# Optimization experiments

Measured on AMD Instinct MI355X. Metric: run time of the kernel, lower is better.

## Reference

```python
import jax, jax.numpy as jnp
import numpy as np

T, MEM, B, DM, N, D = 1024, 1024, 4, 1024, 16, 64
C = MEM + T
SCALE = 1.0 / D ** 0.5
LN_EPS = 1e-5


def _rel_shift(x):
    # x: [T, C, B, N] -> Transformer-XL relative shift
    t, c = x.shape[0], x.shape[1]
    zero_pad = jnp.zeros((t, 1) + x.shape[2:], x.dtype)
    x_padded = jnp.concatenate([zero_pad, x], axis=1)  # [T, C+1, B, N]
    x_padded = x_padded.reshape((c + 1, t) + x.shape[2:])
    return x_padded[1:].reshape(x.shape)


def setup_inputs() -> dict:
    key = jax.random.key(0)
    ks = jax.random.split(key, 8)
    h = jax.random.normal(ks[0], (T, B, DM), jnp.float32)
    m = jax.random.normal(ks[1], (MEM, B, DM), jnp.float32)
    r = jax.random.normal(ks[2], (C, DM), jnp.float32)
    # causal mask with memory: query i (global pos MEM+i) may attend to j <= MEM+i
    mask = (jnp.arange(C)[None, :] > (jnp.arange(T)[:, None] + MEM))[:, :, None]  # [T,C,1] bool, True=disallow
    W_qkv = jax.random.normal(ks[3], (DM, 3 * N * D), jnp.float32) * 0.02
    W_r = jax.random.normal(ks[4], (DM, N * D), jnp.float32) * 0.02
    W_o = jax.random.normal(ks[5], (N * D, DM), jnp.float32) * 0.02
    r_w_bias = jax.random.normal(ks[6], (N, D), jnp.float32)
    r_r_bias = jax.random.normal(ks[7], (N, D), jnp.float32)
    ln_gamma = jnp.ones((DM,), jnp.float32)
    ln_beta = jnp.zeros((DM,), jnp.float32)
    return {"h": h, "m": m, "r": r, "mask": mask, "W_qkv": W_qkv, "W_r": W_r,
            "W_o": W_o, "r_w_bias": r_w_bias, "r_r_bias": r_r_bias,
            "ln_gamma": ln_gamma, "ln_beta": ln_beta}


def reference(h, m, r, mask, W_qkv, W_r, W_o, r_w_bias, r_r_bias, ln_gamma, ln_beta):
    t, b = h.shape[0], h.shape[1]
    c = r.shape[0]
    cat = jnp.concatenate([m, h], axis=0)          # [C, B, DM]
    w_heads = cat @ W_qkv                           # [C, B, 3*N*D]
    w_q, w_k, w_v = jnp.split(w_heads, 3, axis=-1)
    w_q = w_q[-t:].reshape(t, b, N, D)              # [T,B,N,D]
    w_k = w_k.reshape(c, b, N, D)                   # [C,B,N,D]
    w_v = w_v.reshape(c, b, N, D)                   # [C,B,N,D]
    r_k = (r @ W_r).reshape(c, N, D)                # [C,N,D]
    AC = jnp.einsum('ibnd,jbnd->ijbn', w_q + r_w_bias, w_k)
    BD = jnp.einsum('ibnd,jnd->ijbn', w_q + r_r_bias, r_k)
    BD = _rel_shift(BD)
    score = (AC + BD) * SCALE                       # [T,C,B,N]
    score = jnp.where(mask[:, :, :, None], jnp.float32(-65000.0), score.astype(jnp.float32)).astype(score.dtype)
    prob = jax.nn.softmax(score, axis=1)
    vec = jnp.einsum('ijbn,jbnd->ibnd', prob, w_v).reshape(t, b, N * D)
    attn_out = vec @ W_o                            # [T,B,DM]
    x = h + attn_out
    mu = jnp.mean(x, axis=-1, keepdims=True)
    var = jnp.mean((x - mu) ** 2, axis=-1, keepdims=True)
    return (x - mu) * jax.lax.rsqrt(var + LN_EPS) * ln_gamma + ln_beta
```

## Files before the change

### kernel.cpp

```cpp
#include <hip/hip_runtime.h>
#include <stdint.h>

#define T_LEN 1024
#define MEM_LEN 1024
#define C_LEN 2048
#define B_SZ 4
#define DM_ 1024
#define NH 16
#define HD 64

typedef __attribute__((ext_vector_type(8))) short short8;
typedef __attribute__((ext_vector_type(4))) float f32x4;
typedef __attribute__((ext_vector_type(4))) unsigned short ushort4v;
typedef __attribute__((ext_vector_type(4))) float float4v;

__device__ __forceinline__ unsigned short f2bf(float f) {
  union { float f; unsigned int u; } v; v.f = f;
  unsigned int r = v.u + 0x7fffu + ((v.u >> 16) & 1u);
  return (unsigned short)(r >> 16);
}
__device__ __forceinline__ float bf2f(unsigned short b) {
  union { unsigned int u; float f; } v; v.u = ((unsigned int)b) << 16;
  return v.f;
}
__device__ __forceinline__ f32x4 mfma16(short8 a, short8 b, f32x4 c) {
  return __builtin_amdgcn_mfma_f32_16x16x32_bf16(a, b, c, 0, 0, 0);
}

__global__ void k_cat_convert(const float* __restrict__ m, const float* __restrict__ h,
                              unsigned short* __restrict__ outB) {
  int idx = blockIdx.x * 256 + threadIdx.x;
  const int MQ = (MEM_LEN * B_SZ * DM_) / 4;
  float4v v;
  if (idx < MQ) v = ((const float4v*)m)[idx];
  else          v = ((const float4v*)h)[idx - MQ];
  ushort4v o;
  o.x = f2bf(v.x); o.y = f2bf(v.y); o.z = f2bf(v.z); o.w = f2bf(v.w);
  ((ushort4v*)outB)[idx] = o;
}

__global__ void k_f32_to_bf16(const float* __restrict__ in, unsigned short* __restrict__ outB, int nq) {
  int idx = blockIdx.x * 256 + threadIdx.x;
  if (idx >= nq) return;
  float4v v = ((const float4v*)in)[idx];
  ushort4v o;
  o.x = f2bf(v.x); o.y = f2bf(v.y); o.z = f2bf(v.z); o.w = f2bf(v.w);
  ((ushort4v*)outB)[idx] = o;
}

__global__ void k_transpose_bf16(const float* __restrict__ in, unsigned short* __restrict__ out,
                                 int R, int Ccols) {
  __shared__ float tile[32][33];
  int c0 = blockIdx.x * 32, r0 = blockIdx.y * 32;
  int tx = threadIdx.x & 31, ty = threadIdx.x >> 5;
#pragma unroll
  for (int p = 0; p < 4; ++p)
    tile[ty + 8 * p][tx] = in[(size_t)(r0 + ty + 8 * p) * Ccols + c0 + tx];
  __syncthreads();
#pragma unroll
  for (int p = 0; p < 4; ++p)
    out[(size_t)(c0 + ty + 8 * p) * R + r0 + tx] = f2bf(tile[tx][ty + 8 * p]);
}

template <int EPI>
__global__ __launch_bounds__(256) void k_gemm(const unsigned short* __restrict__ A,
                                              const unsigned short* __restrict__ BT,
                                              void* __restrict__ Cout, int M, int N, int K,
                                              int ldc, int col0) {
  __shared__ unsigned short As[128 * 64];
  __shared__ unsigned short Bs[128 * 64];
  const int tid = threadIdx.x;
  const int w = tid >> 6, l = tid & 63;
  const int wm = w >> 1, wn = w & 1;
  const int lg = l >> 4, lr = l & 15;
  const int gx = gridDim.x;
  const int pid = blockIdx.y * gx + blockIdx.x;
  const int xcd = pid & 7;
  const int idx = pid >> 3;
  const int cb = idx % gx;
  const int rb = (idx / gx) * 8 + xcd;
  const int m0 = rb * 128, n0 = cb * 128;
  f32x4 acc[4][4] = {};
  const int lrow8 = l >> 3;
  const int scol = (l & 7) * 8;
  const unsigned short* Abase = A + (size_t)m0 * K;
  const unsigned short* Bbase = BT + (size_t)n0 * K;
  for (int kt = 0; kt < K; kt += 64) {
    __syncthreads();
#pragma unroll
    for (int q = 0; q < 4; ++q) {
      int chunk = w * 4 + q;
      int row = chunk * 8 + lrow8;
      __builtin_amdgcn_global_load_lds(
          (const __attribute__((address_space(1))) void*)(Abase + (size_t)row * K + kt + scol),
          (__attribute__((address_space(3))) void*)(As + chunk * 512), 16, 0, 0);
      __builtin_amdgcn_global_load_lds(
          (const __attribute__((address_space(1))) void*)(Bbase + (size_t)row * K + kt + scol),
          (__attribute__((address_space(3))) void*)(Bs + chunk * 512), 16, 0, 0);
    }
    __syncthreads();
#pragma unroll
    for (int ks = 0; ks < 2; ++ks) {
      short8 a[4], bb[4];
#pragma unroll
      for (int mi = 0; mi < 4; ++mi)
        a[mi] = *(const short8*)&As[(wm * 64 + mi * 16 + lr) * 64 + ks * 32 + lg * 8];
#pragma unroll
      for (int ni = 0; ni < 4; ++ni)
        bb[ni] = *(const short8*)&Bs[(wn * 64 + ni * 16 + lr) * 64 + ks * 32 + lg * 8];
#pragma unroll
      for (int mi = 0; mi < 4; ++mi)
#pragma unroll
        for (int ni = 0; ni < 4; ++ni)
          acc[mi][ni] = mfma16(a[mi], bb[ni], acc[mi][ni]);
    }
  }
#pragma unroll
  for (int mi = 0; mi < 4; ++mi)
#pragma unroll
    for (int ni = 0; ni < 4; ++ni)
#pragma unroll
      for (int r = 0; r < 4; ++r) {
        int row = m0 + wm * 64 + mi * 16 + lg * 4 + r;
        int col = col0 + n0 + wn * 64 + ni * 16 + lr;
        if (EPI == 0)
          ((unsigned short*)Cout)[(size_t)row * ldc + col] = f2bf(acc[mi][ni][r]);
        else
          ((float*)Cout)[(size_t)row * ldc + col] = acc[mi][ni][r];
      }
}

__global__ void k_vt(const unsigned short* __restrict__ wheads, unsigned short* __restrict__ VT) {
  __shared__ unsigned short tile[64][72];
  int c0 = blockIdx.x * 64;
  int n = blockIdx.y, b = blockIdx.z;
  int t = threadIdx.x;
#pragma unroll
  for (int p = 0; p < 16; ++p) {
    int idx = p * 256 + t;
    int r = idx >> 6, d = idx & 63;
    tile[d][r] = wheads[(size_t)((c0 + r) * 4 + b) * 3072 + 2048 + n * 64 + d];
  }
  __syncthreads();
#pragma unroll
  for (int p = 0; p < 16; ++p) {
    int idx = p * 256 + t;
    int d = idx >> 6, c = idx & 63;
    VT[(size_t)((b * 16 + n) * 64 + d) * 2048 + c0 + c] = tile[d][c];
  }
}

__global__ void k_repack(const unsigned short* __restrict__ wheads,
                         const unsigned short* __restrict__ RkG,
                         unsigned short* __restrict__ Kp,
                         unsigned short* __restrict__ Qp,
                         unsigned short* __restrict__ Rkp) {
  int gid = blockIdx.x * 256 + threadIdx.x;
  const int NK = (B_SZ * NH * C_LEN * HD) / 8;
  const int NQ = (B_SZ * NH * T_LEN * HD) / 8;
  if (gid < NK) {
    int d0 = (gid & 7) * 8;
    int c  = (gid >> 3) & 2047;
    int n  = (gid >> 14) & 15;
    int b  = gid >> 18;
    short8 v = *(const short8*)&wheads[(size_t)(c * 4 + b) * 3072 + 1024 + n * 64 + d0];
    *(short8*)&Kp[(size_t)gid * 8] = v;
  } else if (gid < NK + NQ) {
    int g2 = gid - NK;
    int d0 = (g2 & 7) * 8;
    int t  = (g2 >> 3) & 1023;
    int n  = (g2 >> 13) & 15;
    int b  = g2 >> 17;
    short8 v = *(const short8*)&wheads[(size_t)((MEM_LEN + t) * 4 + b) * 3072 + n * 64 + d0];
    *(short8*)&Qp[(size_t)g2 * 8] = v;
  } else {
    int g3 = gid - NK - NQ;
    int d0 = (g3 & 7) * 8;
    int c  = (g3 >> 3) & 2047;
    int n  = g3 >> 14;
    short8 v = *(const short8*)&RkG[(size_t)c * 1024 + n * 64 + d0];
    *(short8*)&Rkp[(size_t)g3 * 8] = v;
  }
}

__global__ void k_bias_dots(const unsigned short* __restrict__ Kp,
                            const unsigned short* __restrict__ Rkp,
                            const float* __restrict__ rwb, const float* __restrict__ rrb,
                            float* __restrict__ uk, float* __restrict__ vr) {
  int gid = blockIdx.x * 256 + threadIdx.x;
  if (gid < B_SZ * NH * C_LEN) {
    int bn = gid >> 11;
    int n = bn & 15;
    const unsigned short* kp = Kp + (size_t)gid * 64;
    float s = 0.f;
#pragma unroll
    for (int q = 0; q < 8; ++q) {
      short8 v = *(const short8*)&kp[q * 8];
#pragma unroll
      for (int e = 0; e < 8; ++e)
        s += bf2f((unsigned short)v[e]) * rwb[n * 64 + q * 8 + e];
    }
    uk[gid] = s;
  } else {
    int g2 = gid - B_SZ * NH * C_LEN;
    int n = g2 >> 11;
    const unsigned short* rp = Rkp + (size_t)g2 * 64;
    float s = 0.f;
#pragma unroll
    for (int q = 0; q < 8; ++q) {
      short8 v = *(const short8*)&rp[q * 8];
#pragma unroll
      for (int e = 0; e < 8; ++e)
        s += bf2f((unsigned short)v[e]) * rrb[n * 64 + q * 8 + e];
    }
    vr[g2] = s;
  }
}

__device__ __forceinline__ void stage_tile(const unsigned short* __restrict__ Kbase,
                                           const unsigned short* __restrict__ Vbase,
                                           unsigned short* ksBuf, unsigned short* vsBuf,
                                           int j0, int tid) {
#pragma unroll
  for (int q = 0; q < 2; ++q) {
    int chunk = q * 256 + tid;
    int row = chunk >> 3;
    int slot = chunk & 7;
    int ss = slot ^ (row & 7);
    __builtin_amdgcn_global_load_lds(
        (const __attribute__((address_space(1))) void*)(Kbase + (size_t)(j0 + row) * 64 + ss * 8),
        (__attribute__((address_space(3))) void*)(ksBuf + chunk * 8), 16, 0, 0);
    __builtin_amdgcn_global_load_lds(
        (const __attribute__((address_space(1))) void*)(Vbase + (size_t)row * 2048 + j0 + ss * 8),
        (__attribute__((address_space(3))) void*)(vsBuf + chunk * 8), 16, 0, 0);
  }
}

__global__ __launch_bounds__(256) void k_attn(const unsigned short* __restrict__ Qp,
                                              const unsigned short* __restrict__ Kp,
                                              const unsigned short* __restrict__ VT,
                                              const unsigned short* __restrict__ Rkp,
                                              const float* __restrict__ uk,
                                              const float* __restrict__ vr,
                                              float* __restrict__ po,
                                              float* __restrict__ psumG) {
  __shared__ __align__(16) unsigned short Ks[2][64 * 64];
  __shared__ __align__(16) unsigned short Vs[2][64 * 64];
  __shared__ unsigned short P[4][16][72];
  const int tid = threadIdx.x;
  const int w = tid >> 6, l = tid & 63;
  const int lg = l >> 4, lr = l & 15;
  const int L = blockIdx.x;
  const int bnlo = L & 7;
  const int rest = L >> 3;
  const int bnhi = rest / 48;
  const int inner = rest - bnhi * 48;
  const int xt = inner / 3;
  const int s  = inner - xt * 3;
  const int bn = bnhi * 8 + bnlo;
  const int i0 = xt * 64;
  const int n = bn & 15, b = bn >> 4;
  const int wrow = i0 + w * 16;

  const int ntile = xt + 17;
  const int t0 = (s * ntile) / 3;
  const int t1 = ((s + 1) * ntile) / 3;

  const unsigned short* Kbase = Kp + (size_t)bn * 2048 * 64;
  const unsigned short* Vbase = VT + (size_t)bn * 64 * 2048;
  const unsigned short* Rkbase = Rkp + (size_t)n * 2048 * 64;

  short8 aq0, aq1;
  {
    const unsigned short* qp = Qp + (size_t)(bn * 1024 + wrow + lr) * 64 + lg * 8;
    aq0 = *(const short8*)qp;
    aq1 = *(const short8*)(qp + 32);
  }
  float psum[4];
  f32x4 o[4];
#pragma unroll
  for (int r = 0; r < 4; ++r) psum[r] = 0.f;
#pragma unroll
  for (int df = 0; df < 4; ++df) o[df] = (f32x4){0.f, 0.f, 0.f, 0.f};

  const float* ukp = uk + (size_t)bn * 2048;
  const float* vrp = vr + (size_t)n * 2048;

  stage_tile(Kbase, Vbase, Ks[0], Vs[0], t0 * 64, tid);
  stage_tile(Kbase, Vbase, Ks[1], Vs[1], (t0 + 1) * 64, tid);

  const float EXPC = 0.18033688011112042f;

  for (int jt = t0; jt < t1; ++jt) {
    const int j0 = jt * 64;
    const int cur = (jt - t0) & 1;
    if (jt + 1 < t1) { asm volatile("s_waitcnt vmcnt(4)" ::: "memory"); }
    else             { asm volatile("s_waitcnt vmcnt(0)" ::: "memory"); }
    __builtin_amdgcn_s_barrier();

    f32x4 sac[4];
#pragma unroll
    for (int jf = 0; jf < 4; ++jf) sac[jf] = (f32x4){0.f, 0.f, 0.f, 0.f};
#pragma unroll
    for (int jf = 0; jf < 4; ++jf) {
      int row = jf * 16 + lr;
      int rx = row & 7;
      short8 k0 = *(const short8*)&Ks[cur][row * 64 + ((lg ^ rx) * 8)];
      short8 k1 = *(const short8*)&Ks[cur][row * 64 + (((4 + lg) ^ rx) * 8)];
      sac[jf] = mfma16(aq0, k0, sac[jf]);
      sac[jf] = mfma16(aq1, k1, sac[jf]);
    }
    const int kbw = j0 + 1008 - i0 - w * 16;
    f32x4 gb[5];
#pragma unroll
    for (int jg = 0; jg < 5; ++jg) {
      int rowK = kbw + jg * 16 + lr;
      short8 b0 = {}, b1 = {};
      float vrv = 0.f;
      if (rowK < C_LEN) {
        const unsigned short* rp = Rkbase + (size_t)rowK * 64 + lg * 8;
        b0 = *(const short8*)rp;
        b1 = *(const short8*)(rp + 32);
        vrv = vrp[rowK];
      }
      f32x4 g = (f32x4){0.f, 0.f, 0.f, 0.f};
      g = mfma16(aq0, b0, g);
      g = mfma16(aq1, b1, g);
#pragma unroll
      for (int r = 0; r < 4; ++r) g[r] += vrv;
      gb[jg] = g;
    }
    float ukv[4];
#pragma unroll
    for (int jf = 0; jf < 4; ++jf) ukv[jf] = ukp[j0 + jf * 16 + lr];
    float p[4][4];
#pragma unroll
    for (int r = 0; r < 4; ++r) {
      const int R = lg * 4 + r;
      const int delta = lr + 15 - R;
      const int src = (l & 48) | (delta & 15);
      float v0 = __shfl(gb[0][r], src);
      float v1 = __shfl(gb[1][r], src);
      float v2 = __shfl(gb[2][r], src);
      float v3 = __shfl(gb[3][r], src);
      float v4 = __shfl(gb[4][r], src);
      const bool hi = delta >= 16;
      float bd0 = hi ? v1 : v0;
      float bd1 = hi ? v2 : v1;
      float bd2 = hi ? v3 : v2;
      float bd3 = hi ? v4 : v3;
      const int jlim = i0 + w * 16 + R + MEM_LEN;
      int j = j0 + lr;
      p[0][r] = (j > jlim) ? 0.f : exp2f((sac[0][r] + bd0 + ukv[0]) * EXPC);
      j += 16;
      p[1][r] = (j > jlim) ? 0.f : exp2f((sac[1][r] + bd1 + ukv[1]) * EXPC);
      j += 16;
      p[2][r] = (j > jlim) ? 0.f : exp2f((sac[2][r] + bd2 + ukv[2]) * EXPC);
      j += 16;
      p[3][r] = (j > jlim) ? 0.f : exp2f((sac[3][r] + bd3 + ukv[3]) * EXPC);
    }
#pragma unroll
    for (int jf = 0; jf < 4; ++jf)
#pragma unroll
      for (int r = 0; r < 4; ++r) psum[r] += p[jf][r];
#pragma unroll
    for (int jf = 0; jf < 4; ++jf)
#pragma unroll
      for (int r = 0; r < 4; ++r)
        P[w][lg * 4 + r][jf * 16 + lr] = f2bf(p[jf][r]);
#pragma unroll
    for (int ks = 0; ks < 2; ++ks) {
      short8 ap = *(const short8*)&P[w][lr][ks * 32 + lg * 8];
#pragma unroll
      for (int df = 0; df < 4; ++df) {
        int row = df * 16 + lr;
        int rx = row & 7;
        short8 vv = *(const short8*)&Vs[cur][row * 64 + (((ks * 4 + lg) ^ rx) * 8)];
        o[df] = mfma16(ap, vv, o[df]);
      }
    }
    __builtin_amdgcn_s_barrier();
    if (jt + 2 < t1)
      stage_tile(Kbase, Vbase, Ks[cur], Vs[cur], (jt + 2) * 64, tid);
  }
  const int pbase = (bn * 16 + xt) * 3 + s;
  float* poB = po + (size_t)pbase * 4096;
#pragma unroll
  for (int r = 0; r < 4; ++r) {
    float v = psum[r];
    v += __shfl_xor(v, 1);
    v += __shfl_xor(v, 2);
    v += __shfl_xor(v, 4);
    v += __shfl_xor(v, 8);
    if (lr == 0) psumG[pbase * 64 + w * 16 + lg * 4 + r] = v;
  }
#pragma unroll
  for (int df = 0; df < 4; ++df)
#pragma unroll
    for (int r = 0; r < 4; ++r)
      poB[(w * 16 + lg * 4 + r) * 64 + df * 16 + lr] = o[df][r];
}

__global__ __launch_bounds__(256) void k_ared(const float* __restrict__ po,
                                              const float* __restrict__ psumG,
                                              unsigned short* __restrict__ vec) {
  const int idx = blockIdx.x;
  const int tid = threadIdx.x;
  const int bn = idx >> 4, xt = idx & 15;
  const int b = bn >> 4, n = bn & 15;
  __shared__ float rs[64];
  if (tid < 64) {
    const float* q = psumG + idx * 192;
    rs[tid] = q[tid] + q[tid + 64] + q[tid + 128];
  }
  __syncthreads();
  const float4v* p0 = (const float4v*)(po + (size_t)(idx * 3 + 0) * 4096);
  const float4v* p1 = (const float4v*)(po + (size_t)(idx * 3 + 1) * 4096);
  const float4v* p2 = (const float4v*)(po + (size_t)(idx * 3 + 2) * 4096);
#pragma unroll
  for (int k = 0; k < 4; ++k) {
    int e = tid + k * 256;
    int row = e >> 4, d4 = e & 15;
    float4v a = p0[e], bb = p1[e], c = p2[e];
    float inv = 1.f / rs[row];
    int t = xt * 64 + row;
    ushort4v ov;
    ov.x = f2bf((a.x + bb.x + c.x) * inv);
    ov.y = f2bf((a.y + bb.y + c.y) * inv);
    ov.z = f2bf((a.z + bb.z + c.z) * inv);
    ov.w = f2bf((a.w + bb.w + c.w) * inv);
    *(ushort4v*)&vec[(size_t)(t * 4 + b) * 1024 + n * 64 + d4 * 4] = ov;
  }
}

__global__ __launch_bounds__(256) void k_ln(const float* __restrict__ xg, const float* __restrict__ h,
                                            const float* __restrict__ gamma, const float* __restrict__ beta,
                                            float* __restrict__ out) {
  const int row = blockIdx.x;
  const int t = threadIdx.x;
  __shared__ float red1[4], red2[4];
  float4v xv = ((const float4v*)(xg + (size_t)row * 1024))[t];
  float4v hv = ((const float4v*)(h + (size_t)row * 1024))[t];
  float x0 = xv.x + hv.x, x1 = xv.y + hv.y, x2 = xv.z + hv.z, x3 = xv.w + hv.w;
  float s = x0 + x1 + x2 + x3;
#pragma unroll
  for (int off = 1; off < 64; off <<= 1) s += __shfl_xor(s, off);
  if ((t & 63) == 0) red1[t >> 6] = s;
  __syncthreads();
  float mean = (red1[0] + red1[1] + red1[2] + red1[3]) * (1.f / 1024.f);
  float d0 = x0 - mean, d1 = x1 - mean, d2 = x2 - mean, d3 = x3 - mean;
  float q = d0 * d0 + d1 * d1 + d2 * d2 + d3 * d3;
#pragma unroll
  for (int off = 1; off < 64; off <<= 1) q += __shfl_xor(q, off);
  if ((t & 63) == 0) red2[t >> 6] = q;
  __syncthreads();
  float var = (red2[0] + red2[1] + red2[2] + red2[3]) * (1.f / 1024.f);
  float rs = rsqrtf(var + 1e-5f);
  float4v gv = ((const float4v*)gamma)[t];
  float4v bv = ((const float4v*)beta)[t];
  float4v ov;
  ov.x = d0 * rs * gv.x + bv.x;
  ov.y = d1 * rs * gv.y + bv.y;
  ov.z = d2 * rs * gv.z + bv.z;
  ov.w = d3 * rs * gv.w + bv.w;
  ((float4v*)(out + (size_t)row * 1024))[t] = ov;
}

extern "C" void kernel_launch(void* const* d_in, const int* in_sizes, int n_in,
                              void* d_out, int out_size, void* d_ws, size_t ws_size,
                              hipStream_t stream) {
  (void)in_sizes; (void)n_in; (void)out_size; (void)ws_size;
  const float* h    = (const float*)d_in[0];
  const float* m    = (const float*)d_in[1];
  const float* r    = (const float*)d_in[2];
  const float* Wqkv = (const float*)d_in[4];
  const float* Wr   = (const float*)d_in[5];
  const float* Wo   = (const float*)d_in[6];
  const float* rwb  = (const float*)d_in[7];
  const float* rrb  = (const float*)d_in[8];
  const float* gam  = (const float*)d_in[9];
  const float* bet  = (const float*)d_in[10];
  float* out = (float*)d_out;

  char* ws = (char*)d_ws;
  unsigned short* catB   = (unsigned short*)(ws + 0);
  unsigned short* WqkvT  = (unsigned short*)(ws + 16777216);
  unsigned short* WrT    = (unsigned short*)(ws + 23068672);
  unsigned short* WoT    = (unsigned short*)(ws + 25165824);
  unsigned short* wheads = (unsigned short*)(ws + 27262976);
  unsigned short* RkG    = (unsigned short*)(ws + 77594624);
  unsigned short* VT     = (unsigned short*)(ws + 81788928);
  float* uk              = (float*)(ws + 98566144);
  float* vr              = (float*)(ws + 99090432);
  unsigned short* vec    = (unsigned short*)(ws + 99221504);
  float* xbuf            = (float*)(ws + 107610112);
  unsigned short* rB     = (unsigned short*)(ws + 124387328);
  unsigned short* Kp     = (unsigned short*)(ws + 128581632);
  unsigned short* Qp     = (unsigned short*)(ws + 145358848);
  unsigned short* Rkp    = (unsigned short*)(ws + 153747456);

  float* po    = (float*)(ws + 27262976);
  float* psumG = (float*)(ws + 124387328);

  hipLaunchKernelGGL(k_cat_convert, dim3(8192), dim3(256), 0, stream, m, h, catB);
  hipLaunchKernelGGL(k_f32_to_bf16, dim3(2048), dim3(256), 0, stream, r, rB, 524288);
  hipLaunchKernelGGL(k_transpose_bf16, dim3(96, 32), dim3(256), 0, stream, Wqkv, WqkvT, 1024, 3072);
  hipLaunchKernelGGL(k_transpose_bf16, dim3(32, 32), dim3(256), 0, stream, Wr, WrT, 1024, 1024);
  hipLaunchKernelGGL(k_transpose_bf16, dim3(32, 32), dim3(256), 0, stream, Wo, WoT, 1024, 1024);
  hipLaunchKernelGGL(k_gemm<0>, dim3(16, 64), dim3(256), 0, stream,
                     catB, WqkvT + (size_t)1024 * 1024, (void*)wheads, 8192, 2048, 1024, 3072, 1024);
  hipLaunchKernelGGL(k_gemm<0>, dim3(8, 32), dim3(256), 0, stream,
                     catB + (size_t)4096 * 1024, WqkvT, (void*)(wheads + (size_t)4096 * 3072),
                     4096, 1024, 1024, 3072, 0);
  hipLaunchKernelGGL(k_gemm<0>, dim3(8, 16), dim3(256), 0, stream, rB, WrT, (void*)RkG, 2048, 1024, 1024, 1024, 0);
  hipLaunchKernelGGL(k_vt, dim3(32, 16, 4), dim3(256), 0, stream, wheads, VT);
  hipLaunchKernelGGL(k_repack, dim3(7168), dim3(256), 0, stream, wheads, RkG, Kp, Qp, Rkp);
  hipLaunchKernelGGL(k_bias_dots, dim3(640), dim3(256), 0, stream, Kp, Rkp, rwb, rrb, uk, vr);
  hipLaunchKernelGGL(k_attn, dim3(3072), dim3(256), 0, stream, Qp, Kp, VT, Rkp, uk, vr, po, psumG);
  hipLaunchKernelGGL(k_ared, dim3(1024), dim3(256), 0, stream, po, psumG, vec);
  hipLaunchKernelGGL(k_gemm<1>, dim3(8, 32), dim3(256), 0, stream, vec, WoT, (void*)xbuf, 4096, 1024, 1024, 1024, 0);
  hipLaunchKernelGGL(k_ln, dim3(4096), dim3(256), 0, stream, xbuf, h, gam, bet, out);
}
```

Before: 359.1 us.

## Fuse head-major repacking into GEMM epilogues and store attention partials as bf16

The QKV and R projection GEMMs now write K, V, Q and R_k straight into per-head [b,n,c,d] layouts from their epilogues. This removes the separate k_repack kernel and the intermediate wheads/RkG buffers, along with one full read and write of those tensors. The attention kernel's split-KV partial outputs are also stored as bf16 instead of fp32, halving that traffic into the reduction kernel at some cost in accumulation precision. The epilogue stores are scalar 2-byte writes scattered by head, which may coalesce worse than before.

```diff
diff --git a/kernel.cpp b/kernel.cpp
--- a/kernel.cpp
+++ b/kernel.cpp
@@ -62,11 +62,11 @@
     out[(size_t)(c0 + ty + 8 * p) * R + r0 + tx] = f2bf(tile[tx][ty + 8 * p]);
 }
 
-template <int EPI>
+template <int MODE>
 __global__ __launch_bounds__(256) void k_gemm(const unsigned short* __restrict__ A,
                                               const unsigned short* __restrict__ BT,
-                                              void* __restrict__ Cout, int M, int N, int K,
-                                              int ldc, int col0) {
+                                              void* __restrict__ out1, void* __restrict__ out2,
+                                              int M, int N, int K, int ldc) {
   __shared__ unsigned short As[128 * 64];
   __shared__ unsigned short Bs[128 * 64];
   const int tid = threadIdx.x;
@@ -122,24 +122,38 @@
 #pragma unroll
       for (int r = 0; r < 4; ++r) {
         int row = m0 + wm * 64 + mi * 16 + lg * 4 + r;
-        int col = col0 + n0 + wn * 64 + ni * 16 + lr;
-        if (EPI == 0)
-          ((unsigned short*)Cout)[(size_t)row * ldc + col] = f2bf(acc[mi][ni][r]);
-        else
-          ((float*)Cout)[(size_t)row * ldc + col] = acc[mi][ni][r];
+        int cc = n0 + wn * 64 + ni * 16 + lr;
+        float val = acc[mi][ni][r];
+        if (MODE == 1) {
+          ((float*)out1)[(size_t)row * ldc + cc] = val;
+        } else if (MODE == 2) {
+          int nn = (cc & 1023) >> 6, d = cc & 63;
+          int c = row >> 2, b = row & 3;
+          size_t addr = ((size_t)((b * 16 + nn) * 2048 + c)) * 64 + d;
+          unsigned short* dst = (cc < 1024) ? (unsigned short*)out1 : (unsigned short*)out2;
+          dst[addr] = f2bf(val);
+        } else if (MODE == 3) {
+          int nn = cc >> 6, d = cc & 63;
+          int t = row >> 2, b = row & 3;
+          ((unsigned short*)out1)[((size_t)((b * 16 + nn) * 1024 + t)) * 64 + d] = f2bf(val);
+        } else {
+          int nn = cc >> 6, d = cc & 63;
+          ((unsigned short*)out1)[((size_t)(nn * 2048 + row)) * 64 + d] = f2bf(val);
+        }
       }
 }
 
-__global__ void k_vt(const unsigned short* __restrict__ wheads, unsigned short* __restrict__ VT) {
+__global__ void k_vt(const unsigned short* __restrict__ Vp, unsigned short* __restrict__ VT) {
   __shared__ unsigned short tile[64][72];
   int c0 = blockIdx.x * 64;
   int n = blockIdx.y, b = blockIdx.z;
   int t = threadIdx.x;
+  const unsigned short* src = Vp + ((size_t)((b * 16 + n) * 2048 + c0)) * 64;
 #pragma unroll
   for (int p = 0; p < 16; ++p) {
     int idx = p * 256 + t;
     int r = idx >> 6, d = idx & 63;
-    tile[d][r] = wheads[(size_t)((c0 + r) * 4 + b) * 3072 + 2048 + n * 64 + d];
+    tile[d][r] = src[(size_t)r * 64 + d];
   }
   __syncthreads();
 #pragma unroll
@@ -147,39 +161,6 @@
     int idx = p * 256 + t;
     int d = idx >> 6, c = idx & 63;
     VT[(size_t)((b * 16 + n) * 64 + d) * 2048 + c0 + c] = tile[d][c];
-  }
-}
-
-__global__ void k_repack(const unsigned short* __restrict__ wheads,
-                         const unsigned short* __restrict__ RkG,
-                         unsigned short* __restrict__ Kp,
-                         unsigned short* __restrict__ Qp,
-                         unsigned short* __restrict__ Rkp) {
-  int gid = blockIdx.x * 256 + threadIdx.x;
-  const int NK = (B_SZ * NH * C_LEN * HD) / 8;
-  const int NQ = (B_SZ * NH * T_LEN * HD) / 8;
-  if (gid < NK) {
-    int d0 = (gid & 7) * 8;
-    int c  = (gid >> 3) & 2047;
-    int n  = (gid >> 14) & 15;
-    int b  = gid >> 18;
-    short8 v = *(const short8*)&wheads[(size_t)(c * 4 + b) * 3072 + 1024 + n * 64 + d0];
-    *(short8*)&Kp[(size_t)gid * 8] = v;
-  } else if (gid < NK + NQ) {
-    int g2 = gid - NK;
-    int d0 = (g2 & 7) * 8;
-    int t  = (g2 >> 3) & 1023;
-    int n  = (g2 >> 13) & 15;
-    int b  = g2 >> 17;
-    short8 v = *(const short8*)&wheads[(size_t)((MEM_LEN + t) * 4 + b) * 3072 + n * 64 + d0];
-    *(short8*)&Qp[(size_t)g2 * 8] = v;
-  } else {
-    int g3 = gid - NK - NQ;
-    int d0 = (g3 & 7) * 8;
-    int c  = (g3 >> 3) & 2047;
-    int n  = g3 >> 14;
-    short8 v = *(const short8*)&RkG[(size_t)c * 1024 + n * 64 + d0];
-    *(short8*)&Rkp[(size_t)g3 * 8] = v;
   }
 }
 
@@ -242,7 +223,7 @@
                                               const unsigned short* __restrict__ Rkp,
                                               const float* __restrict__ uk,
                                               const float* __restrict__ vr,
-                                              float* __restrict__ po,
+                                              unsigned short* __restrict__ po,
                                               float* __restrict__ psumG) {
   __shared__ __align__(16) unsigned short Ks[2][64 * 64];
   __shared__ __align__(16) unsigned short Vs[2][64 * 64];
@@ -384,7 +365,7 @@
       stage_tile(Kbase, Vbase, Ks[cur], Vs[cur], (jt + 2) * 64, tid);
   }
   const int pbase = (bn * 16 + xt) * 3 + s;
-  float* poB = po + (size_t)pbase * 4096;
+  unsigned short* poB = po + (size_t)pbase * 4096;
 #pragma unroll
   for (int r = 0; r < 4; ++r) {
     float v = psum[r];
@@ -398,10 +379,10 @@
   for (int df = 0; df < 4; ++df)
 #pragma unroll
     for (int r = 0; r < 4; ++r)
-      poB[(w * 16 + lg * 4 + r) * 64 + df * 16 + lr] = o[df][r];
-}
-
-__global__ __launch_bounds__(256) void k_ared(const float* __restrict__ po,
+      poB[(w * 16 + lg * 4 + r) * 64 + df * 16 + lr] = f2bf(o[df][r]);
+}
+
+__global__ __launch_bounds__(256) void k_ared(const unsigned short* __restrict__ po,
                                               const float* __restrict__ psumG,
                                               unsigned short* __restrict__ vec) {
   const int idx = blockIdx.x;
@@ -414,21 +395,21 @@
     rs[tid] = q[tid] + q[tid + 64] + q[tid + 128];
   }
   __syncthreads();
-  const float4v* p0 = (const float4v*)(po + (size_t)(idx * 3 + 0) * 4096);
-  const float4v* p1 = (const float4v*)(po + (size_t)(idx * 3 + 1) * 4096);
-  const float4v* p2 = (const float4v*)(po + (size_t)(idx * 3 + 2) * 4096);
+  const ushort4v* p0 = (const ushort4v*)(po + (size_t)(idx * 3 + 0) * 4096);
+  const ushort4v* p1 = (const ushort4v*)(po + (size_t)(idx * 3 + 1) * 4096);
+  const ushort4v* p2 = (const ushort4v*)(po + (size_t)(idx * 3 + 2) * 4096);
 #pragma unroll
   for (int k = 0; k < 4; ++k) {
     int e = tid + k * 256;
     int row = e >> 4, d4 = e & 15;
-    float4v a = p0[e], bb = p1[e], c = p2[e];
+    ushort4v a = p0[e], bb = p1[e], c = p2[e];
     float inv = 1.f / rs[row];
     int t = xt * 64 + row;
     ushort4v ov;
-    ov.x = f2bf((a.x + bb.x + c.x) * inv);
-    ov.y = f2bf((a.y + bb.y + c.y) * inv);
-    ov.z = f2bf((a.z + bb.z + c.z) * inv);
-    ov.w = f2bf((a.w + bb.w + c.w) * inv);
+    ov.x = f2bf((bf2f(a.x) + bf2f(bb.x) + bf2f(c.x)) * inv);
+    ov.y = f2bf((bf2f(a.y) + bf2f(bb.y) + bf2f(c.y)) * inv);
+    ov.z = f2bf((bf2f(a.z) + bf2f(bb.z) + bf2f(c.z)) * inv);
+    ov.w = f2bf((bf2f(a.w) + bf2f(bb.w) + bf2f(c.w)) * inv);
     *(ushort4v*)&vec[(size_t)(t * 4 + b) * 1024 + n * 64 + d4 * 4] = ov;
   }
 }
@@ -487,8 +468,8 @@
   unsigned short* WqkvT  = (unsigned short*)(ws + 16777216);
   unsigned short* WrT    = (unsigned short*)(ws + 23068672);
   unsigned short* WoT    = (unsigned short*)(ws + 25165824);
-  unsigned short* wheads = (unsigned short*)(ws + 27262976);
-  unsigned short* RkG    = (unsigned short*)(ws + 77594624);
+  unsigned short* Vp     = (unsigned short*)(ws + 27262976);
+  unsigned short* po     = (unsigned short*)(ws + 44040192);
   unsigned short* VT     = (unsigned short*)(ws + 81788928);
   float* uk              = (float*)(ws + 98566144);
   float* vr              = (float*)(ws + 99090432);
@@ -498,8 +479,6 @@
   unsigned short* Kp     = (unsigned short*)(ws + 128581632);
   unsigned short* Qp     = (unsigned short*)(ws + 145358848);
   unsigned short* Rkp    = (unsigned short*)(ws + 153747456);
-
-  float* po    = (float*)(ws + 27262976);
   float* psumG = (float*)(ws + 124387328);
 
   hipLaunchKernelGGL(k_cat_convert, dim3(8192), dim3(256), 0, stream, m, h, catB);
@@ -507,17 +486,17 @@
   hipLaunchKernelGGL(k_transpose_bf16, dim3(96, 32), dim3(256), 0, stream, Wqkv, WqkvT, 1024, 3072);
   hipLaunchKernelGGL(k_transpose_bf16, dim3(32, 32), dim3(256), 0, stream, Wr, WrT, 1024, 1024);
   hipLaunchKernelGGL(k_transpose_bf16, dim3(32, 32), dim3(256), 0, stream, Wo, WoT, 1024, 1024);
-  hipLaunchKernelGGL(k_gemm<0>, dim3(16, 64), dim3(256), 0, stream,
-                     catB, WqkvT + (size_t)1024 * 1024, (void*)wheads, 8192, 2048, 1024, 3072, 1024);
-  hipLaunchKernelGGL(k_gemm<0>, dim3(8, 32), dim3(256), 0, stream,
-                     catB + (size_t)4096 * 1024, WqkvT, (void*)(wheads + (size_t)4096 * 3072),
-                     4096, 1024, 1024, 3072, 0);
-  hipLaunchKernelGGL(k_gemm<0>, dim3(8, 16), dim3(256), 0, stream, rB, WrT, (void*)RkG, 2048, 1024, 1024, 1024, 0);
-  hipLaunchKernelGGL(k_vt, dim3(32, 16, 4), dim3(256), 0, stream, wheads, VT);
-  hipLaunchKernelGGL(k_repack, dim3(7168), dim3(256), 0, stream, wheads, RkG, Kp, Qp, Rkp);
+  hipLaunchKernelGGL(k_gemm<2>, dim3(16, 64), dim3(256), 0, stream,
+                     catB, WqkvT + (size_t)1024 * 1024, (void*)Kp, (void*)Vp, 8192, 2048, 1024, 0);
+  hipLaunchKernelGGL(k_gemm<3>, dim3(8, 32), dim3(256), 0, stream,
+                     catB + (size_t)4096 * 1024, WqkvT, (void*)Qp, nullptr, 4096, 1024, 1024, 0);
+  hipLaunchKernelGGL(k_gemm<4>, dim3(8, 16), dim3(256), 0, stream,
+                     rB, WrT, (void*)Rkp, nullptr, 2048, 1024, 1024, 0);
+  hipLaunchKernelGGL(k_vt, dim3(32, 16, 4), dim3(256), 0, stream, Vp, VT);
   hipLaunchKernelGGL(k_bias_dots, dim3(640), dim3(256), 0, stream, Kp, Rkp, rwb, rrb, uk, vr);
   hipLaunchKernelGGL(k_attn, dim3(3072), dim3(256), 0, stream, Qp, Kp, VT, Rkp, uk, vr, po, psumG);
   hipLaunchKernelGGL(k_ared, dim3(1024), dim3(256), 0, stream, po, psumG, vec);
-  hipLaunchKernelGGL(k_gemm<1>, dim3(8, 32), dim3(256), 0, stream, vec, WoT, (void*)xbuf, 4096, 1024, 1024, 1024, 0);
+  hipLaunchKernelGGL(k_gemm<1>, dim3(8, 32), dim3(256), 0, stream,
+                     vec, WoT, (void*)xbuf, nullptr, 4096, 1024, 1024, 1024);
   hipLaunchKernelGGL(k_ln, dim3(4096), dim3(256), 0, stream, xbuf, h, gam, bet, out);
 }
```

Result: faster. 345.1 us (-3.9%).
